# Optimization experiments

Hardware: AMD Instinct MI355X
Metric: run time of the kernel (lower is better)

## Reference

```python
import jax, jax.numpy as jnp
import numpy as np

B, CIN, HALF, H, W = 4, 3, 32, 512, 512
K_MODE, PAD_MODE, N_LEVELS = 11, 5, 17  # 11x11 mode window, reflect pad 5, round(x*255/16) in 0..16
SLOPE, EPS = 0.01, 1e-5


def _leaky(x):
    return jnp.where(x > 0, x, SLOPE * x)


def _bn(x, g, b):
    # BatchNorm2d in training mode: batch statistics over (B,H,W), biased var
    m = x.mean(axis=(0, 2, 3), keepdims=True)
    v = x.var(axis=(0, 2, 3), keepdims=True)
    return (x - m) * jax.lax.rsqrt(v + EPS) * g[None, :, None, None] + b[None, :, None, None]


def _mode_pool(x):
    # quantize to 17 discrete levels, then sliding-window histogram mode (fused
    # equivalent of unfold + torch.mode; argmax first-hit == smallest tied value)
    k = jnp.clip(jnp.round(x * (255.0 / 16.0)), 0, N_LEVELS - 1).astype(jnp.int32)
    kp = jnp.pad(k, ((0, 0), (0, 0), (PAD_MODE, PAD_MODE), (PAD_MODE, PAD_MODE)), mode='reflect')
    onehot = (kp[..., None] == jnp.arange(N_LEVELS, dtype=jnp.int32)).astype(jnp.float32)
    counts = jax.lax.reduce_window(onehot, 0.0, jax.lax.add,
                                   (1, 1, K_MODE, K_MODE, 1), (1, 1, 1, 1, 1), 'VALID')
    mode_k = jnp.argmax(counts, axis=-1)  # [B,C,H,W]
    return mode_k.astype(jnp.float32) * (16.0 / 256.0)


def _nearest(x, Ho, Wo):
    # torch interpolate(mode='nearest'): src = floor(dst * in/out)
    hi, wi = x.shape[2], x.shape[3]
    ri = (jnp.arange(Ho) * hi) // Ho
    ci = (jnp.arange(Wo) * wi) // Wo
    return x[:, :, ri][:, :, :, ci]


def _forward(x, w1, b1, w2, b2, bn1_g, bn1_b, w3, b3, bn2_g, bn2_b,
             k_down, k_w, bnw_g, bnw_b, k_h, bnh_g, bnh_b):
    xm = _mode_pool(x)  # [B,CIN,H,W]
    # prepare: 1x1 conv -> LeakyReLU -> 1x1 conv -> BN -> LeakyReLU -> depthwise 1x1 -> BN -> LeakyReLU
    h = _leaky(jnp.einsum('bchw,oc->bohw', xm, w1) + b1[None, :, None, None])
    h = jnp.einsum('bchw,oc->bohw', h, w2) + b2[None, :, None, None]
    h = _leaky(_bn(h, bn1_g, bn1_b))
    h = h * w3[None, :, None, None] + b3[None, :, None, None]  # groups=half 1x1 conv
    h = _leaky(_bn(h, bn2_g, bn2_b))
    Bs, half, Ho, Wo = h.shape
    score = jnp.zeros((Bs, 2 * half, Ho, Wo), jnp.float32)
    d = h
    while min(d.shape[2], d.shape[3]) >= 3:  # static pyramid: 512->171->57->19->7->3->1
        d = jax.lax.conv_general_dilated(d, k_down, (3, 3), ((1, 1), (1, 1)),
                                         dimension_numbers=('NCHW', 'OIHW', 'NCHW'),
                                         feature_group_count=half)
        z = _nearest(d, Ho, Wo)
        wbr = _leaky(_bn(z * k_w[None, :, None, None], bnw_g, bnw_b))  # width branch (SharedConv k=1, no bias)
        hbr = _leaky(_bn(z * k_h[None, :, None, None], bnh_g, bnh_b))  # height branch
        # stack(dim=1).reshape => width channels first, then height channels
        score = score + jnp.concatenate([wbr, hbr], axis=1)
    return score


def setup_inputs():
    key = jax.random.key(0)
    ks = jax.random.split(key, 8)
    x = jax.random.uniform(ks[0], (B, CIN, H, W), dtype=jnp.float32)
    s1, s2 = 1.0 / np.sqrt(CIN), 1.0 / np.sqrt(2 * CIN)
    return {
        'x': x,
        'w1': jax.random.uniform(ks[1], (2 * CIN, CIN), jnp.float32, -s1, s1),
        'b1': jax.random.uniform(ks[2], (2 * CIN,), jnp.float32, -s1, s1),
        'w2': jax.random.uniform(ks[3], (HALF, 2 * CIN), jnp.float32, -s2, s2),
        'b2': jax.random.uniform(ks[4], (HALF,), jnp.float32, -s2, s2),
        'bn1_g': jnp.ones((HALF,), jnp.float32),
        'bn1_b': jnp.zeros((HALF,), jnp.float32),
        'w3': jax.random.uniform(ks[5], (HALF,), jnp.float32, -1.0, 1.0),
        'b3': jax.random.uniform(ks[6], (HALF,), jnp.float32, -1.0, 1.0),
        'bn2_g': jnp.ones((HALF,), jnp.float32),
        'bn2_b': jnp.zeros((HALF,), jnp.float32),
        'k_down': jnp.full((HALF, 1, 3, 3), 0.5, jnp.float32),  # SharedConv init
        'k_w': jnp.full((HALF,), 0.5, jnp.float32),
        'bnw_g': jnp.ones((HALF,), jnp.float32),
        'bnw_b': jnp.zeros((HALF,), jnp.float32),
        'k_h': jnp.full((HALF,), 0.5, jnp.float32),
        'bnh_g': jnp.ones((HALF,), jnp.float32),
        'bnh_b': jnp.zeros((HALF,), jnp.float32),
    }


def reference(x, w1, b1, w2, b2, bn1_g, bn1_b, w3, b3, bn2_g, bn2_b,
              k_down, k_w, bnw_g, bnw_b, k_h, bnh_g, bnh_b):
    return _forward(x, w1, b1, w2, b2, bn1_g, bn1_b, w3, b3, bn2_g, bn2_b,
                    k_down, k_w, bnw_g, bnw_b, k_h, bnh_g, bnh_b)
```

## Files before the change

### kernel.cpp

```cpp
#include <hip/hip_runtime.h>

#define HH 512
#define WW 512
#define HW 262144
#define NPIX 1048576
#define NPIXF 1048576.0f

typedef float f4 __attribute__((ext_vector_type(4)));

__device__ __forceinline__ float leaky(float v) { return v > 0.f ? v : 0.01f * v; }

__device__ __forceinline__ float repw(int i, int s) {
    return (float)(((i + 1) * 512 + s - 1) / s - (i * 512 + s - 1) / s);
}

__device__ __forceinline__ void hins(unsigned long long& h0, unsigned long long& h1,
                                     unsigned& c16, int val) {
    unsigned long long inc = 1ull << ((val & 7) * 8);
    h0 += (val < 8) ? inc : 0;
    h1 += (val >= 8 && val < 16) ? inc : 0;
    c16 += (unsigned)(val >> 4);
}
__device__ __forceinline__ void hrem(unsigned long long& h0, unsigned long long& h1,
                                     unsigned& c16, int val) {
    unsigned long long inc = 1ull << ((val & 7) * 8);
    h0 -= (val < 8) ? inc : 0;
    h1 -= (val >= 8 && val < 16) ? inc : 0;
    c16 -= (unsigned)(val >> 4);
}

__global__ __launch_bounds__(256) void mode_kernel(const float* __restrict__ x,
                                                   unsigned char* __restrict__ modeq) {
    __shared__ unsigned char q[26 * 272];
    __shared__ unsigned ch[2][267 * 5];
    const int plane = blockIdx.z;
    const int tc0 = blockIdx.x * 256;
    const int tr0 = blockIdx.y * 16;
    const float* xp = x + (size_t)plane * HW;
    for (int idx = threadIdx.x; idx < 26 * 266; idx += 256) {
        int r = idx / 266;
        int cc = idx - r * 266;
        int gr = tr0 + r - 5; gr = gr < 0 ? -gr : (gr > 511 ? 1022 - gr : gr);
        int gc = tc0 + cc - 5; gc = gc < 0 ? -gc : (gc > 511 ? 1022 - gc : gc);
        float v = rintf(xp[gr * WW + gc] * 15.9375f);
        v = fminf(fmaxf(v, 0.f), 16.f);
        q[r * 272 + cc] = (unsigned char)(int)v;
    }
    const int t = threadIdx.x;
    unsigned long long A0 = 0, A1 = 0; unsigned A2 = 0;
    unsigned long long B0 = 0, B1 = 0; unsigned B2 = 0;
    __syncthreads();
    for (int r = 0; r < 16; ++r) {
        if (r == 0) {
            #pragma unroll
            for (int v = 0; v < 11; ++v) {
                hins(A0, A1, A2, q[v * 272 + t]);
                if (t < 10) hins(B0, B1, B2, q[v * 272 + 256 + t]);
            }
        } else {
            hrem(A0, A1, A2, q[(r - 1) * 272 + t]);
            hins(A0, A1, A2, q[(r + 10) * 272 + t]);
            if (t < 10) {
                hrem(B0, B1, B2, q[(r - 1) * 272 + 256 + t]);
                hins(B0, B1, B2, q[(r + 10) * 272 + 256 + t]);
            }
        }
        unsigned* cb = ch[r & 1];
        cb[t * 5 + 0] = (unsigned)A0;
        cb[t * 5 + 1] = (unsigned)(A0 >> 32);
        cb[t * 5 + 2] = (unsigned)A1;
        cb[t * 5 + 3] = (unsigned)(A1 >> 32);
        cb[t * 5 + 4] = A2;
        if (t < 10) {
            cb[(256 + t) * 5 + 0] = (unsigned)B0;
            cb[(256 + t) * 5 + 1] = (unsigned)(B0 >> 32);
            cb[(256 + t) * 5 + 2] = (unsigned)B1;
            cb[(256 + t) * 5 + 3] = (unsigned)(B1 >> 32);
            cb[(256 + t) * 5 + 4] = B2;
        }
        __syncthreads();
        unsigned long long H0 = 0, H1 = 0; unsigned C = 0;
        #pragma unroll
        for (int v = 0; v < 11; ++v) {
            const unsigned* p = &cb[(t + v) * 5];
            H0 += (unsigned long long)p[0] | ((unsigned long long)p[1] << 32);
            H1 += (unsigned long long)p[2] | ((unsigned long long)p[3] << 32);
            C += p[4];
        }
        unsigned m = 0;
        #pragma unroll
        for (int i = 0; i < 8; ++i) {
            unsigned cnt = (unsigned)(H0 >> (8 * i)) & 0xFFu;
            unsigned val = (cnt << 8) | (unsigned)(16 - i);
            m = m > val ? m : val;
        }
        #pragma unroll
        for (int i = 8; i < 16; ++i) {
            unsigned cnt = (unsigned)(H1 >> (8 * (i - 8))) & 0xFFu;
            unsigned val = (cnt << 8) | (unsigned)(16 - i);
            m = m > val ? m : val;
        }
        unsigned val16 = (C << 8);
        m = m > val16 ? m : val16;
        int k = 16 - (int)(m & 0xFFu);
        modeq[(size_t)plane * HW + (size_t)(tr0 + r) * WW + tc0 + t] = (unsigned char)k;
    }
}

__global__ __launch_bounds__(256) void hist_kernel(const unsigned char* __restrict__ modeq,
                                                   const float* __restrict__ w1,
                                                   const float* __restrict__ b1,
                                                   unsigned* __restrict__ partial,
                                                   float* __restrict__ mpart) {
    __shared__ unsigned lh[4913];
    __shared__ float mred[27][4];
    for (int i = threadIdx.x; i < 4913; i += 256) lh[i] = 0;
    __syncthreads();
    int base = blockIdx.x * 8192;
    int b = base >> 18;
    int hw0 = base & (HW - 1);
    const unsigned char* mp = modeq + (size_t)b * 3 * HW;
    #pragma unroll
    for (int j = 0; j < 8; ++j) {
        int g = threadIdx.x + 256 * j;
        int hw = hw0 + g * 4;
        unsigned u0 = *(const unsigned*)(mp + hw);
        unsigned u1 = *(const unsigned*)(mp + hw + HW);
        unsigned u2 = *(const unsigned*)(mp + hw + 2 * HW);
        #pragma unroll
        for (int k = 0; k < 4; ++k) {
            int k0 = (u0 >> (8 * k)) & 0xFF;
            int k1 = (u1 >> (8 * k)) & 0xFF;
            int k2 = (u2 >> (8 * k)) & 0xFF;
            atomicAdd(&lh[k0 + 17 * k1 + 289 * k2], 1u);
        }
    }
    __syncthreads();
    unsigned* pp = partial + blockIdx.x * 4913;
    for (int i = threadIdx.x; i < 4913; i += 256) pp[i] = lh[i];
    float w1r[18], b1r[6];
    #pragma unroll
    for (int k = 0; k < 18; ++k) w1r[k] = w1[k];
    #pragma unroll
    for (int o = 0; o < 6; ++o) b1r[o] = b1[o];
    float M[27];
    #pragma unroll
    for (int i = 0; i < 27; ++i) M[i] = 0.f;
    for (int bin = threadIdx.x; bin < 4913; bin += 256) {
        float cnt = (float)lh[bin];
        int k0 = bin % 17;
        int r = bin / 17;
        int k1 = r % 17;
        int k2 = r / 17;
        float xm0 = k0 * 0.0625f, xm1 = k1 * 0.0625f, xm2 = k2 * 0.0625f;
        float t1[6];
        #pragma unroll
        for (int o = 0; o < 6; ++o)
            t1[o] = leaky(xm0 * w1r[o * 3] + xm1 * w1r[o * 3 + 1] + xm2 * w1r[o * 3 + 2] + b1r[o]);
        #pragma unroll
        for (int o = 0; o < 6; ++o) M[o] += cnt * t1[o];
        int ii = 6;
        #pragma unroll
        for (int j = 0; j < 6; ++j)
            #pragma unroll
            for (int k = j; k < 6; ++k) { M[ii] += cnt * t1[j] * t1[k]; ++ii; }
    }
    int wv = threadIdx.x >> 6;
    #pragma unroll
    for (int i = 0; i < 27; ++i) {
        float v = M[i];
        #pragma unroll
        for (int off = 32; off >= 1; off >>= 1) v += __shfl_xor(v, off);
        if ((threadIdx.x & 63) == 0) mred[i][wv] = v;
    }
    __syncthreads();
    if (threadIdx.x < 27)
        mpart[blockIdx.x * 27 + threadIdx.x] =
            mred[threadIdx.x][0] + mred[threadIdx.x][1] +
            mred[threadIdx.x][2] + mred[threadIdx.x][3];
}

__global__ __launch_bounds__(256) void solveBF_kernel(const float* __restrict__ mpart,
                                                      const unsigned* __restrict__ partial,
                                                      const float* __restrict__ w1,
                                                      const float* __restrict__ b1,
                                                      const float* __restrict__ w2,
                                                      const float* __restrict__ b2,
                                                      const float* __restrict__ g1,
                                                      const float* __restrict__ bb1,
                                                      float* __restrict__ p1g,
                                                      float* __restrict__ tpart) {
    __shared__ float red[8][32];
    __shared__ float mom[27];
    __shared__ float a1s[32], c1s[32];
    __shared__ float rs[8][32], rq[8][32];
    const int t = threadIdx.x;
    const int c = t & 31;
    const int sub = t >> 5;
    {
        float s = 0.f;
        if (c < 27) {
            #pragma unroll
            for (int j = 0; j < 16; ++j) s += mpart[(sub * 16 + j) * 27 + c];
        }
        red[sub][c] = s;
    }
    __syncthreads();
    if (t < 27) {
        float v = 0.f;
        #pragma unroll
        for (int g = 0; g < 8; ++g) v += red[g][t];
        mom[t] = v;
    }
    __syncthreads();
    if (t < 32) {
        float w2r[6];
        #pragma unroll
        for (int k = 0; k < 6; ++k) w2r[k] = w2[t * 6 + k];
        float b2c = b2[t];
        float wm1 = 0.f;
        #pragma unroll
        for (int k = 0; k < 6; ++k) wm1 += w2r[k] * mom[k];
        float q = 0.f;
        int ii = 6;
        #pragma unroll
        for (int j = 0; j < 6; ++j)
            #pragma unroll
            for (int k = j; k < 6; ++k) {
                float f = w2r[j] * w2r[k] * mom[ii];
                q += (j == k) ? f : 2.f * f;
                ++ii;
            }
        float mean = b2c + wm1 / NPIXF;
        float ex2 = b2c * b2c + 2.f * b2c * (wm1 / NPIXF) + q / NPIXF;
        float var = ex2 - mean * mean;
        float a = g1[t] * rsqrtf(var + 1e-5f);
        a1s[t] = a;
        c1s[t] = bb1[t] - mean * a;
        if (blockIdx.x == 0) { p1g[t] = a; p1g[32 + t] = c1s[t]; }
    }
    __syncthreads();
    float w1r[18], b1r[6];
    #pragma unroll
    for (int k = 0; k < 18; ++k) w1r[k] = w1[k];
    #pragma unroll
    for (int o = 0; o < 6; ++o) b1r[o] = b1[o];
    float w2r[6];
    #pragma unroll
    for (int k = 0; k < 6; ++k) w2r[k] = w2[c * 6 + k];
    float b2c = b2[c];
    float a1 = a1s[c], c1 = c1s[c];
    float sm = 0.f, sq = 0.f;
    for (int bin = blockIdx.x + 32 * sub; bin < 4913; bin += 256) {
        unsigned cs = 0;
        const unsigned* pb = partial + bin;
        #pragma unroll
        for (int j = 0; j < 4; ++j) cs += pb[(size_t)(c + 32 * j) * 4913];
        #pragma unroll
        for (int off = 16; off >= 1; off >>= 1) cs += __shfl_xor((int)cs, off);
        float cnt = (float)cs;
        int k0 = bin % 17;
        int r = bin / 17;
        int k1 = r % 17;
        int k2 = r / 17;
        float xm0 = k0 * 0.0625f, xm1 = k1 * 0.0625f, xm2 = k2 * 0.0625f;
        float t1[6];
        #pragma unroll
        for (int o = 0; o < 6; ++o)
            t1[o] = leaky(xm0 * w1r[o * 3] + xm1 * w1r[o * 3 + 1] + xm2 * w1r[o * 3 + 2] + b1r[o]);
        float h2 = b2c;
        #pragma unroll
        for (int k = 0; k < 6; ++k) h2 += w2r[k] * t1[k];
        float tt = leaky(a1 * h2 + c1);
        sm += cnt * tt;
        sq += cnt * tt * tt;
    }
    rs[sub][c] = sm; rq[sub][c] = sq;
    __syncthreads();
    if (t < 32) {
        float s = 0.f, qq = 0.f;
        #pragma unroll
        for (int g = 0; g < 8; ++g) { s += rs[g][t]; qq += rq[g][t]; }
        tpart[blockIdx.x * 64 + t] = s;
        tpart[blockIdx.x * 64 + 32 + t] = qq;
    }
}

__global__ void fin2_kernel(const float* __restrict__ tpart, const float* __restrict__ w3,
                            const float* __restrict__ b3, const float* __restrict__ g,
                            const float* __restrict__ bb, float* __restrict__ p2) {
    int c = threadIdx.x;
    float s = 0.f, qq = 0.f;
    #pragma unroll
    for (int k = 0; k < 32; ++k) { s += tpart[k * 64 + c]; qq += tpart[k * 64 + 32 + c]; }
    float mt = s / NPIXF;
    float vt = qq / NPIXF - mt * mt;
    float m2 = w3[c] * mt + b3[c];
    float v2 = w3[c] * w3[c] * vt;
    float a = g[c] * rsqrtf(v2 + 1e-5f);
    p2[c] = a;
    p2[32 + c] = bb[c] - m2 * a;
}

__global__ __launch_bounds__(64) void d1_kernel(const unsigned char* __restrict__ modeq,
                                                const float* __restrict__ w1,
                                                const float* __restrict__ b1,
                                                const float* __restrict__ w2,
                                                const float* __restrict__ b2,
                                                const float* __restrict__ w3,
                                                const float* __restrict__ b3,
                                                const float* __restrict__ p1,
                                                const float* __restrict__ p2,
                                                const float* __restrict__ kd,
                                                float* __restrict__ d1) {
    int j = blockIdx.x * 64 + threadIdx.x;
    if (j >= 171) return;
    int i = blockIdx.y;
    int b = blockIdx.z;
    float acc[32];
    #pragma unroll
    for (int c = 0; c < 32; ++c) acc[c] = 0.f;
    const unsigned char* mp = modeq + (size_t)b * 3 * HW;
    #pragma unroll
    for (int u = 0; u < 3; ++u) {
        int r = 3 * i - 1 + u;
        if (r < 0 || r > 511) continue;
        #pragma unroll
        for (int v = 0; v < 3; ++v) {
            int col = 3 * j - 1 + v;
            if (col < 0 || col > 511) continue;
            int off = r * WW + col;
            float xm0 = mp[off] * 0.0625f, xm1 = mp[off + HW] * 0.0625f, xm2 = mp[off + 2 * HW] * 0.0625f;
            float t1[6];
            #pragma unroll
            for (int o = 0; o < 6; ++o)
                t1[o] = leaky(xm0 * w1[o * 3] + xm1 * w1[o * 3 + 1] + xm2 * w1[o * 3 + 2] + b1[o]);
            #pragma unroll
            for (int c = 0; c < 32; ++c) {
                float h2 = b2[c];
                #pragma unroll
                for (int k = 0; k < 6; ++k) h2 += w2[c * 6 + k] * t1[k];
                float t = leaky(h2 * p1[c] + p1[32 + c]);
                float uu = t * w3[c] + b3[c];
                float hv = leaky(uu * p2[c] + p2[32 + c]);
                acc[c] += hv * kd[c * 9 + u * 3 + v];
            }
        }
    }
    size_t base = ((size_t)(b * 32) * 171 + i) * 171 + j;
    #pragma unroll
    for (int c = 0; c < 32; ++c) d1[base + (size_t)c * 29241] = acc[c];
}

__device__ __forceinline__ void red_store(float sm, float sq, float* rsc, float* ps) {
    #pragma unroll
    for (int off = 32; off >= 1; off >>= 1) {
        sm += __shfl_xor(sm, off);
        sq += __shfl_xor(sq, off);
    }
    __syncthreads();
    int wv = threadIdx.x >> 6;
    if ((threadIdx.x & 63) == 0) { rsc[wv] = sm; rsc[8 + wv] = sq; }
    __syncthreads();
    if (threadIdx.x == 0) {
        ps[0] = rsc[0] + rsc[1] + rsc[2] + rsc[3];
        ps[1] = rsc[8] + rsc[9] + rsc[10] + rsc[11];
    }
}

__device__ __forceinline__ void lvl(const float* src, int sin, float* dstL,
                                    float* dstG, int sout, const float* kreg,
                                    float* rsc, float* ps) {
    float sm = 0.f, sq = 0.f;
    int n = sout * sout;
    for (int i = threadIdx.x; i < n; i += 256) {
        int oi = i / sout, oj = i - oi * sout;
        float acc = 0.f;
        #pragma unroll
        for (int u = 0; u < 3; ++u) {
            int r = 3 * oi - 1 + u;
            if ((unsigned)r >= (unsigned)sin) continue;
            #pragma unroll
            for (int v = 0; v < 3; ++v) {
                int cc = 3 * oj - 1 + v;
                if ((unsigned)cc >= (unsigned)sin) continue;
                acc += src[r * sin + cc] * kreg[u * 3 + v];
            }
        }
        dstG[i] = acc;
        if (dstL) dstL[i] = acc;
        float w = repw(oi, sout) * repw(oj, sout);
        sm += w * acc;
        sq += w * acc * acc;
    }
    red_store(sm, sq, rsc, ps);
}

__global__ __launch_bounds__(256) void pyramid_kernel(const float* __restrict__ d1,
                                                      float* __restrict__ d2,
                                                      float* __restrict__ d3,
                                                      float* __restrict__ d4,
                                                      float* __restrict__ d5,
                                                      float* __restrict__ d6,
                                                      const float* __restrict__ kd,
                                                      float* __restrict__ pstats) {
    __shared__ float buf2[3249];
    __shared__ float buf3[361];
    __shared__ float buf4[49];
    __shared__ float buf5[9];
    __shared__ float rsc[16];
    int bc = blockIdx.x;
    int c = bc & 31;
    float kreg[9];
    #pragma unroll
    for (int qq = 0; qq < 9; ++qq) kreg[qq] = kd[c * 9 + qq];
    float* ps = pstats + (size_t)bc * 12;
    const float* s1 = d1 + (size_t)bc * 29241;
    float sm = 0.f, sq = 0.f;
    for (int i = threadIdx.x; i < 29241; i += 256) {
        int oi = i / 171, oj = i - oi * 171;
        float w = repw(oi, 171) * repw(oj, 171);
        float v = s1[i];
        sm += w * v;
        sq += w * v * v;
    }
    red_store(sm, sq, rsc, ps + 0);
    lvl(s1, 171, buf2, d2 + (size_t)bc * 3249, 57, kreg, rsc, ps + 2);
    lvl(buf2, 57, buf3, d3 + (size_t)bc * 361, 19, kreg, rsc, ps + 4);
    lvl(buf3, 19, buf4, d4 + (size_t)bc * 49, 7, kreg, rsc, ps + 6);
    lvl(buf4, 7, buf5, d5 + (size_t)bc * 9, 3, kreg, rsc, ps + 8);
    lvl(buf5, 3, nullptr, d6 + bc, 1, kreg, rsc, ps + 10);
}

__global__ __launch_bounds__(256) void final_kernel(const float* __restrict__ d1,
                                                    const float* __restrict__ d2,
                                                    const float* __restrict__ d3,
                                                    const float* __restrict__ d4,
                                                    const float* __restrict__ d5,
                                                    const float* __restrict__ d6,
                                                    const float* __restrict__ pstats,
                                                    const float* __restrict__ kw,
                                                    const float* __restrict__ gw,
                                                    const float* __restrict__ bw,
                                                    const float* __restrict__ kh,
                                                    const float* __restrict__ gh,
                                                    const float* __restrict__ bh,
                                                    float* __restrict__ out) {
    __shared__ float la[6][4];
    int idx = blockIdx.x * 256 + threadIdx.x;
    int c = (idx >> 16) & 31;
    int b = idx >> 21;
    if (threadIdx.x < 6) {
        int l = threadIdx.x;
        float sm = 0.f, sq = 0.f;
        #pragma unroll
        for (int b4 = 0; b4 < 4; ++b4) {
            const float* ps = pstats + (size_t)(b4 * 32 + c) * 12 + 2 * l;
            sm += ps[0];
            sq += ps[1];
        }
        float mz = sm / NPIXF;
        float vz = sq / NPIXF - mz * mz;
        float kwc = kw[c];
        float aw = gw[c] * rsqrtf(kwc * kwc * vz + 1e-5f);
        float khc = kh[c];
        float ah = gh[c] * rsqrtf(khc * khc * vz + 1e-5f);
        la[l][0] = kwc * aw;
        la[l][1] = bw[c] - kwc * mz * aw;
        la[l][2] = khc * ah;
        la[l][3] = bh[c] - khc * mz * ah;
    }
    __syncthreads();
    int w4 = (idx & 127) << 2;
    int h = (idx >> 7) & 511;
    const float* ds[6] = {d1, d2, d3, d4, d5, d6};
    const int ss[6] = {171, 57, 19, 7, 3, 1};
    float accw[4] = {0.f, 0.f, 0.f, 0.f};
    float acch[4] = {0.f, 0.f, 0.f, 0.f};
    #pragma unroll
    for (int l = 0; l < 6; ++l) {
        int s = ss[l];
        int sh = (h * s) >> 9;
        const float* base = ds[l] + ((size_t)(b * 32 + c) * s + sh) * s;
        float a0 = la[l][0], a1 = la[l][1], a2 = la[l][2], a3 = la[l][3];
        #pragma unroll
        for (int k = 0; k < 4; ++k) {
            int sw = ((w4 + k) * s) >> 9;
            float val = base[sw];
            accw[k] += leaky(val * a0 + a1);
            acch[k] += leaky(val * a2 + a3);
        }
    }
    size_t o = (((size_t)(b * 64 + c)) << 18) + ((size_t)h << 9) + w4;
    f4 vw = {accw[0], accw[1], accw[2], accw[3]};
    f4 vh = {acch[0], acch[1], acch[2], acch[3]};
    __builtin_nontemporal_store(vw, (f4*)(out + o));
    __builtin_nontemporal_store(vh, (f4*)(out + o + (((size_t)32) << 18)));
}

extern "C" void kernel_launch(void* const* d_in, const int* in_sizes, int n_in,
                              void* d_out, int out_size, void* d_ws, size_t ws_size,
                              hipStream_t stream) {
    const float* x     = (const float*)d_in[0];
    const float* w1    = (const float*)d_in[1];
    const float* b1    = (const float*)d_in[2];
    const float* w2    = (const float*)d_in[3];
    const float* b2    = (const float*)d_in[4];
    const float* bn1g  = (const float*)d_in[5];
    const float* bn1b  = (const float*)d_in[6];
    const float* w3    = (const float*)d_in[7];
    const float* b3    = (const float*)d_in[8];
    const float* bn2g  = (const float*)d_in[9];
    const float* bn2b  = (const float*)d_in[10];
    const float* kd    = (const float*)d_in[11];
    const float* kw    = (const float*)d_in[12];
    const float* bnwg  = (const float*)d_in[13];
    const float* bnwb  = (const float*)d_in[14];
    const float* kh    = (const float*)d_in[15];
    const float* bnhg  = (const float*)d_in[16];
    const float* bnhb  = (const float*)d_in[17];
    float* out = (float*)d_out;

    char* ws = (char*)d_ws;
    unsigned char* modeq = (unsigned char*)ws;
    float* mpart  = (float*)(ws + 3145728);
    float* tpart  = (float*)(ws + 3145728 + 13824);
    float* pstats = (float*)(ws + 3145728 + 13824 + 8192);
    float* p1 = (float*)(ws + 3174400);
    float* p2 = p1 + 64;
    unsigned* partial = (unsigned*)(ws + 3174912);
    float* d1 = (float*)(ws + 3174912 + 2515456);
    float* d2 = d1 + 3742848;
    float* d3 = d2 + 415872;
    float* d4 = d3 + 46208;
    float* d5 = d4 + 6272;
    float* d6 = d5 + 1152;

    mode_kernel<<<dim3(2, 32, 12), 256, 0, stream>>>(x, modeq);
    hist_kernel<<<128, 256, 0, stream>>>(modeq, w1, b1, partial, mpart);
    solveBF_kernel<<<32, 256, 0, stream>>>(mpart, partial, w1, b1, w2, b2,
                                           bn1g, bn1b, p1, tpart);
    fin2_kernel<<<1, 32, 0, stream>>>(tpart, w3, b3, bn2g, bn2b, p2);
    d1_kernel<<<dim3(3, 171, 4), 64, 0, stream>>>(modeq, w1, b1, w2, b2, w3, b3, p1, p2, kd, d1);
    pyramid_kernel<<<128, 256, 0, stream>>>(d1, d2, d3, d4, d5, d6, kd, pstats);
    final_kernel<<<32768, 256, 0, stream>>>(d1, d2, d3, d4, d5, d6, pstats,
                                            kw, bnwg, bnwb, kh, bnhg, bnhb, out);
}
```

Measured before the change: 482.7 us.

## Fold moment reduction into solve kernel and fuse BN2 finalize into d1 kernel

The histogram kernel now only writes per-block histograms. Each solve block reduces all 128 partial histograms into a shared float histogram, computes the first and second moments itself, and reuses that histogram in its second pass. The single-thread fin2 kernel is removed, and every d1 block recomputes the BN2 scale and shift from tpart in shared memory. This drops one launch and the mpart round trip, but each of the 32 solve blocks now redundantly reads all partials (about 2.5 MB) and every d1 block repeats the small finalize.

```diff
diff --git a/kernel.cpp b/kernel.cpp
--- a/kernel.cpp
+++ b/kernel.cpp
@@ -108,12 +108,8 @@
 }
 
 __global__ __launch_bounds__(256) void hist_kernel(const unsigned char* __restrict__ modeq,
-                                                   const float* __restrict__ w1,
-                                                   const float* __restrict__ b1,
-                                                   unsigned* __restrict__ partial,
-                                                   float* __restrict__ mpart) {
+                                                   unsigned* __restrict__ partial) {
     __shared__ unsigned lh[4913];
-    __shared__ float mred[27][4];
     for (int i = threadIdx.x; i < 4913; i += 256) lh[i] = 0;
     __syncthreads();
     int base = blockIdx.x * 8192;
@@ -138,50 +134,9 @@
     __syncthreads();
     unsigned* pp = partial + blockIdx.x * 4913;
     for (int i = threadIdx.x; i < 4913; i += 256) pp[i] = lh[i];
-    float w1r[18], b1r[6];
-    #pragma unroll
-    for (int k = 0; k < 18; ++k) w1r[k] = w1[k];
-    #pragma unroll
-    for (int o = 0; o < 6; ++o) b1r[o] = b1[o];
-    float M[27];
-    #pragma unroll
-    for (int i = 0; i < 27; ++i) M[i] = 0.f;
-    for (int bin = threadIdx.x; bin < 4913; bin += 256) {
-        float cnt = (float)lh[bin];
-        int k0 = bin % 17;
-        int r = bin / 17;
-        int k1 = r % 17;
-        int k2 = r / 17;
-        float xm0 = k0 * 0.0625f, xm1 = k1 * 0.0625f, xm2 = k2 * 0.0625f;
-        float t1[6];
-        #pragma unroll
-        for (int o = 0; o < 6; ++o)
-            t1[o] = leaky(xm0 * w1r[o * 3] + xm1 * w1r[o * 3 + 1] + xm2 * w1r[o * 3 + 2] + b1r[o]);
-        #pragma unroll
-        for (int o = 0; o < 6; ++o) M[o] += cnt * t1[o];
-        int ii = 6;
-        #pragma unroll
-        for (int j = 0; j < 6; ++j)
-            #pragma unroll
-            for (int k = j; k < 6; ++k) { M[ii] += cnt * t1[j] * t1[k]; ++ii; }
-    }
-    int wv = threadIdx.x >> 6;
-    #pragma unroll
-    for (int i = 0; i < 27; ++i) {
-        float v = M[i];
-        #pragma unroll
-        for (int off = 32; off >= 1; off >>= 1) v += __shfl_xor(v, off);
-        if ((threadIdx.x & 63) == 0) mred[i][wv] = v;
-    }
-    __syncthreads();
-    if (threadIdx.x < 27)
-        mpart[blockIdx.x * 27 + threadIdx.x] =
-            mred[threadIdx.x][0] + mred[threadIdx.x][1] +
-            mred[threadIdx.x][2] + mred[threadIdx.x][3];
-}
-
-__global__ __launch_bounds__(256) void solveBF_kernel(const float* __restrict__ mpart,
-                                                      const unsigned* __restrict__ partial,
+}
+
+__global__ __launch_bounds__(256) void solveBF_kernel(const unsigned* __restrict__ partial,
                                                       const float* __restrict__ w1,
                                                       const float* __restrict__ b1,
                                                       const float* __restrict__ w2,
@@ -190,28 +145,57 @@
                                                       const float* __restrict__ bb1,
                                                       float* __restrict__ p1g,
                                                       float* __restrict__ tpart) {
-    __shared__ float red[8][32];
+    __shared__ float histf[4913];
+    __shared__ float mred[27][4];
     __shared__ float mom[27];
     __shared__ float a1s[32], c1s[32];
     __shared__ float rs[8][32], rq[8][32];
     const int t = threadIdx.x;
     const int c = t & 31;
     const int sub = t >> 5;
-    {
-        float s = 0.f;
-        if (c < 27) {
+    for (int bin = t; bin < 4913; bin += 256) {
+        unsigned s = 0;
+        for (int blk = 0; blk < 128; ++blk) s += partial[blk * 4913 + bin];
+        histf[bin] = (float)s;
+    }
+    float w1r[18], b1r[6];
+    #pragma unroll
+    for (int k = 0; k < 18; ++k) w1r[k] = w1[k];
+    #pragma unroll
+    for (int o = 0; o < 6; ++o) b1r[o] = b1[o];
+    __syncthreads();
+    float M[27];
+    #pragma unroll
+    for (int i = 0; i < 27; ++i) M[i] = 0.f;
+    for (int bin = t; bin < 4913; bin += 256) {
+        float cnt = histf[bin];
+        int k0 = bin % 17;
+        int r = bin / 17;
+        int k1 = r % 17;
+        int k2 = r / 17;
+        float xm0 = k0 * 0.0625f, xm1 = k1 * 0.0625f, xm2 = k2 * 0.0625f;
+        float t1[6];
+        #pragma unroll
+        for (int o = 0; o < 6; ++o)
+            t1[o] = leaky(xm0 * w1r[o * 3] + xm1 * w1r[o * 3 + 1] + xm2 * w1r[o * 3 + 2] + b1r[o]);
+        #pragma unroll
+        for (int o = 0; o < 6; ++o) M[o] += cnt * t1[o];
+        int ii = 6;
+        #pragma unroll
+        for (int j = 0; j < 6; ++j)
             #pragma unroll
-            for (int j = 0; j < 16; ++j) s += mpart[(sub * 16 + j) * 27 + c];
-        }
-        red[sub][c] = s;
-    }
-    __syncthreads();
-    if (t < 27) {
-        float v = 0.f;
-        #pragma unroll
-        for (int g = 0; g < 8; ++g) v += red[g][t];
-        mom[t] = v;
-    }
+            for (int k = j; k < 6; ++k) { M[ii] += cnt * t1[j] * t1[k]; ++ii; }
+    }
+    int wv = t >> 6;
+    #pragma unroll
+    for (int i = 0; i < 27; ++i) {
+        float v = M[i];
+        #pragma unroll
+        for (int off = 32; off >= 1; off >>= 1) v += __shfl_xor(v, off);
+        if ((t & 63) == 0) mred[i][wv] = v;
+    }
+    __syncthreads();
+    if (t < 27) mom[t] = mred[t][0] + mred[t][1] + mred[t][2] + mred[t][3];
     __syncthreads();
     if (t < 32) {
         float w2r[6];
@@ -240,11 +224,6 @@
         if (blockIdx.x == 0) { p1g[t] = a; p1g[32 + t] = c1s[t]; }
     }
     __syncthreads();
-    float w1r[18], b1r[6];
-    #pragma unroll
-    for (int k = 0; k < 18; ++k) w1r[k] = w1[k];
-    #pragma unroll
-    for (int o = 0; o < 6; ++o) b1r[o] = b1[o];
     float w2r[6];
     #pragma unroll
     for (int k = 0; k < 6; ++k) w2r[k] = w2[c * 6 + k];
@@ -252,13 +231,7 @@
     float a1 = a1s[c], c1 = c1s[c];
     float sm = 0.f, sq = 0.f;
     for (int bin = blockIdx.x + 32 * sub; bin < 4913; bin += 256) {
-        unsigned cs = 0;
-        const unsigned* pb = partial + bin;
-        #pragma unroll
-        for (int j = 0; j < 4; ++j) cs += pb[(size_t)(c + 32 * j) * 4913];
-        #pragma unroll
-        for (int off = 16; off >= 1; off >>= 1) cs += __shfl_xor((int)cs, off);
-        float cnt = (float)cs;
+        float cnt = histf[bin];
         int k0 = bin % 17;
         int r = bin / 17;
         int k1 = r % 17;
@@ -284,22 +257,6 @@
         tpart[blockIdx.x * 64 + t] = s;
         tpart[blockIdx.x * 64 + 32 + t] = qq;
     }
-}
-
-__global__ void fin2_kernel(const float* __restrict__ tpart, const float* __restrict__ w3,
-                            const float* __restrict__ b3, const float* __restrict__ g,
-                            const float* __restrict__ bb, float* __restrict__ p2) {
-    int c = threadIdx.x;
-    float s = 0.f, qq = 0.f;
-    #pragma unroll
-    for (int k = 0; k < 32; ++k) { s += tpart[k * 64 + c]; qq += tpart[k * 64 + 32 + c]; }
-    float mt = s / NPIXF;
-    float vt = qq / NPIXF - mt * mt;
-    float m2 = w3[c] * mt + b3[c];
-    float v2 = w3[c] * w3[c] * vt;
-    float a = g[c] * rsqrtf(v2 + 1e-5f);
-    p2[c] = a;
-    p2[32 + c] = bb[c] - m2 * a;
 }
 
 __global__ __launch_bounds__(64) void d1_kernel(const unsigned char* __restrict__ modeq,
@@ -310,9 +267,26 @@
                                                 const float* __restrict__ w3,
                                                 const float* __restrict__ b3,
                                                 const float* __restrict__ p1,
-                                                const float* __restrict__ p2,
+                                                const float* __restrict__ tpart,
+                                                const float* __restrict__ g2,
+                                                const float* __restrict__ bb2,
                                                 const float* __restrict__ kd,
                                                 float* __restrict__ d1) {
+    __shared__ float p2s[64];
+    if (threadIdx.x < 32) {
+        int c = threadIdx.x;
+        float s = 0.f, qq = 0.f;
+        #pragma unroll
+        for (int k = 0; k < 32; ++k) { s += tpart[k * 64 + c]; qq += tpart[k * 64 + 32 + c]; }
+        float mt = s / NPIXF;
+        float vt = qq / NPIXF - mt * mt;
+        float m2 = w3[c] * mt + b3[c];
+        float v2 = w3[c] * w3[c] * vt;
+        float a = g2[c] * rsqrtf(v2 + 1e-5f);
+        p2s[c] = a;
+        p2s[32 + c] = bb2[c] - m2 * a;
+    }
+    __syncthreads();
     int j = blockIdx.x * 64 + threadIdx.x;
     if (j >= 171) return;
     int i = blockIdx.y;
@@ -342,7 +316,7 @@
                 for (int k = 0; k < 6; ++k) h2 += w2[c * 6 + k] * t1[k];
                 float t = leaky(h2 * p1[c] + p1[32 + c]);
                 float uu = t * w3[c] + b3[c];
-                float hv = leaky(uu * p2[c] + p2[32 + c]);
+                float hv = leaky(uu * p2s[c] + p2s[32 + c]);
                 acc[c] += hv * kd[c * 9 + u * 3 + v];
             }
         }
@@ -523,13 +497,11 @@
 
     char* ws = (char*)d_ws;
     unsigned char* modeq = (unsigned char*)ws;
-    float* mpart  = (float*)(ws + 3145728);
-    float* tpart  = (float*)(ws + 3145728 + 13824);
-    float* pstats = (float*)(ws + 3145728 + 13824 + 8192);
-    float* p1 = (float*)(ws + 3174400);
-    float* p2 = p1 + 64;
-    unsigned* partial = (unsigned*)(ws + 3174912);
-    float* d1 = (float*)(ws + 3174912 + 2515456);
+    float* tpart  = (float*)(ws + 3145728);
+    float* pstats = (float*)(ws + 3145728 + 8192);
+    float* p1 = (float*)(ws + 3160064);
+    unsigned* partial = (unsigned*)(ws + 3160320);
+    float* d1 = (float*)(ws + 3160320 + 2515456);
     float* d2 = d1 + 3742848;
     float* d3 = d2 + 415872;
     float* d4 = d3 + 46208;
@@ -537,11 +509,11 @@
     float* d6 = d5 + 1152;
 
     mode_kernel<<<dim3(2, 32, 12), 256, 0, stream>>>(x, modeq);
-    hist_kernel<<<128, 256, 0, stream>>>(modeq, w1, b1, partial, mpart);
-    solveBF_kernel<<<32, 256, 0, stream>>>(mpart, partial, w1, b1, w2, b2,
+    hist_kernel<<<128, 256, 0, stream>>>(modeq, partial);
+    solveBF_kernel<<<32, 256, 0, stream>>>(partial, w1, b1, w2, b2,
                                            bn1g, bn1b, p1, tpart);
-    fin2_kernel<<<1, 32, 0, stream>>>(tpart, w3, b3, bn2g, bn2b, p2);
-    d1_kernel<<<dim3(3, 171, 4), 64, 0, stream>>>(modeq, w1, b1, w2, b2, w3, b3, p1, p2, kd, d1);
+    d1_kernel<<<dim3(3, 171, 4), 64, 0, stream>>>(modeq, w1, b1, w2, b2, w3, b3,
+                                                  p1, tpart, bn2g, bn2b, kd, d1);
     pyramid_kernel<<<128, 256, 0, stream>>>(d1, d2, d3, d4, d5, d6, kd, pstats);
     final_kernel<<<32768, 256, 0, stream>>>(d1, d2, d3, d4, d5, d6, pstats,
                                             kw, bnwg, bnwb, kh, bnhg, bnhb, out);
```

New measurement: 528.4 us. 1.09x slower.
